# Optimization experiments

Measured on AMD Instinct MI355X. Metric: run time of the kernel, lower is better.

## Reference

```python
import jax, jax.numpy as jnp
import numpy as np

T = 4096
D_MODEL = 1024
H = 16          # n_heads
HD = 64         # head_dim = d_model // n_heads
LW = 64         # local_window
LT = 16         # latent_tokens
CHUNK = 32      # remote_chunk_size


def setup_inputs() -> dict:
    key = jax.random.key(0)
    ks = jax.random.split(key, 11)
    s = 0.02
    return {
        "x":  jax.random.normal(ks[0], (T, D_MODEL), dtype=jnp.float32),
        "Wq": jax.random.normal(ks[1], (D_MODEL, D_MODEL), dtype=jnp.float32) * s,
        "bq": jnp.zeros((D_MODEL,), dtype=jnp.float32),
        "Wk": jax.random.normal(ks[2], (D_MODEL, D_MODEL), dtype=jnp.float32) * s,
        "bk": jnp.zeros((D_MODEL,), dtype=jnp.float32),
        "Wv": jax.random.normal(ks[3], (D_MODEL, D_MODEL), dtype=jnp.float32) * s,
        "bv": jnp.zeros((D_MODEL,), dtype=jnp.float32),
        "Wo": jax.random.normal(ks[4], (D_MODEL, D_MODEL), dtype=jnp.float32) * s,
        "bo": jnp.zeros((D_MODEL,), dtype=jnp.float32),
        "Wg": jax.random.normal(ks[5], (H, D_MODEL), dtype=jnp.float32) * s,
        "bg": jnp.zeros((H,), dtype=jnp.float32),
    }


def reference(x, Wq, bq, Wk, bk, Wv, bv, Wo, bo, Wg, bg):
    """Runs prefill: forward_step for each token, returning per-step outputs [T, D_MODEL].

    Local cache = circular FIFO of size LW (append + pop-oldest == ring overwrite;
    softmax is permutation-invariant so slot order is irrelevant).
    Evicted tokens accumulate in pending sums; every CHUNK evictions the mean k/v
    is written into the remote latent ring of size LT (oldest overwritten).
    Attention happens BEFORE appending the current token's k/v, matching the torch code.
    """
    scale = 1.0 / np.sqrt(HD)
    Tn = x.shape[0]
    Q = (x @ Wq.T + bq).reshape(Tn, H, HD)
    K = (x @ Wk.T + bk).reshape(Tn, H, HD)
    V = (x @ Wv.T + bv).reshape(Tn, H, HD)
    G = jax.nn.sigmoid(x @ Wg.T + bg)  # [T, H] simple gate

    z = lambda *s: jnp.zeros(s, dtype=x.dtype)
    init = (z(LW, H, HD), z(LW, H, HD),   # local k/v ring
            z(LT, H, HD), z(LT, H, HD),   # remote k/v ring
            z(H, HD), z(H, HD),           # pending k/v sums
            jnp.int32(0), jnp.int32(0))   # pending count, remote count

    def step(carry, inp):
        lk, lv, rk, rv, pks, pvs, pc, rc = carry
        q, k, v, g, t = inp
        # ---- local attention over filled slots (count = min(t, LW)) ----
        lvalid = jnp.arange(LW) < jnp.minimum(t, LW)
        ls = jnp.einsum('hd,nhd->hn', q, lk) * scale
        ls = jnp.where(lvalid[None, :], ls, -1e30)
        lo = jnp.einsum('hn,nhd->hd', jax.nn.softmax(ls, axis=-1), lv)
        lo = lo * (t > 0)
        # ---- remote (compressed latent) attention ----
        rvalid = jnp.arange(LT) < jnp.minimum(rc, LT)
        rs = jnp.einsum('hd,nhd->hn', q, rk) * scale
        rs = jnp.where(rvalid[None, :], rs, -1e30)
        ro = jnp.einsum('hn,nhd->hd', jax.nn.softmax(rs, axis=-1), rv)
        ro = ro * (rc > 0)
        # ---- gate and combine ----
        gate = g[:, None]
        out = gate * lo + (1.0 - gate) * ro  # [H, HD]
        # ---- append k/v: ring write evicts token t-LW into pending ----
        pos = jnp.mod(t, LW)
        evict = (t >= LW)
        pks = pks + jnp.where(evict, lk[pos], 0.0)
        pvs = pvs + jnp.where(evict, lv[pos], 0.0)
        pc = pc + evict.astype(jnp.int32)
        lk = lk.at[pos].set(k)
        lv = lv.at[pos].set(v)
        # ---- compress pending into remote ring when CHUNK reached ----
        comp = (pc == CHUNK)
        ridx = jnp.mod(rc, LT)
        rk = jnp.where(comp, rk.at[ridx].set(pks / CHUNK), rk)
        rv = jnp.where(comp, rv.at[ridx].set(pvs / CHUNK), rv)
        rc = rc + comp.astype(jnp.int32)
        pks = jnp.where(comp, 0.0, pks)
        pvs = jnp.where(comp, 0.0, pvs)
        pc = jnp.where(comp, 0, pc)
        return (lk, lv, rk, rv, pks, pvs, pc, rc), out

    ts = jnp.arange(Tn, dtype=jnp.int32)
    _, outs = jax.lax.scan(step, init, (Q, K, V, G, ts))
    return outs.reshape(Tn, D_MODEL) @ Wo.T + bo
```

## Files before the change

kernel.cpp:

```cpp
#include <hip/hip_runtime.h>
#include <hip/hip_bf16.h>
#include <math.h>

typedef __attribute__((ext_vector_type(8))) short short8;
typedef __attribute__((ext_vector_type(4))) float f32x4;

#define TT 4096
#define DM 1024
#define NH 16
#define HD 64
#define PSTR 168

typedef __attribute__((address_space(3))) unsigned int lds_u32;
typedef __attribute__((address_space(1))) unsigned int glb_u32;

__device__ __forceinline__ void async_cp16(const void* g, void* l) {
    __builtin_amdgcn_global_load_lds((glb_u32*)g, (lds_u32*)l, 16, 0, 0);
}

__device__ __forceinline__ float bf2f(unsigned short u) {
    union { unsigned int i; float f; } v;
    v.i = (unsigned int)u << 16;
    return v.f;
}

__global__ __launch_bounds__(256) void cast_all(
    const float* __restrict__ x,  const float* __restrict__ wq,
    const float* __restrict__ wk, const float* __restrict__ wv,
    const float* __restrict__ wo, const float* __restrict__ wg,
    __hip_bfloat16* __restrict__ xb,  __hip_bfloat16* __restrict__ wqb,
    __hip_bfloat16* __restrict__ wkb, __hip_bfloat16* __restrict__ wvb,
    __hip_bfloat16* __restrict__ wob, __hip_bfloat16* __restrict__ wgb)
{
    int b = blockIdx.x;
    const float* src;
    __hip_bfloat16* dst;
    size_t base;
    if (b < 4096)      { src = x;  dst = xb;  base = (size_t)b * 1024; }
    else if (b < 5120) { src = wq; dst = wqb; base = (size_t)(b - 4096) * 1024; }
    else if (b < 6144) { src = wk; dst = wkb; base = (size_t)(b - 5120) * 1024; }
    else if (b < 7168) { src = wv; dst = wvb; base = (size_t)(b - 6144) * 1024; }
    else if (b < 8192) { src = wo; dst = wob; base = (size_t)(b - 7168) * 1024; }
    else               { src = wg; dst = wgb; base = (size_t)(b - 8192) * 1024; }
    size_t i = base + (size_t)threadIdx.x * 4;
    float4 v = *(const float4*)(src + i);
    __hip_bfloat16 h0 = (__hip_bfloat16)v.x;
    __hip_bfloat16 h1 = (__hip_bfloat16)v.y;
    __hip_bfloat16 h2 = (__hip_bfloat16)v.z;
    __hip_bfloat16 h3 = (__hip_bfloat16)v.w;
    ushort4 u;
    u.x = *(unsigned short*)&h0;
    u.y = *(unsigned short*)&h1;
    u.z = *(unsigned short*)&h2;
    u.w = *(unsigned short*)&h3;
    *(ushort4*)((unsigned short*)dst + i) = u;
}

template <typename OutT>
__global__ __launch_bounds__(512, 2) void gemm256(
    const __hip_bfloat16* __restrict__ A,
    const __hip_bfloat16* __restrict__ B0, const __hip_bfloat16* __restrict__ B1,
    const __hip_bfloat16* __restrict__ B2,
    const float* __restrict__ c0, const float* __restrict__ c1, const float* __restrict__ c2,
    OutT* __restrict__ O0, OutT* __restrict__ O1, OutT* __restrict__ O2)
{
    const int K  = DM;
    const int NT = 16;
    __shared__ __align__(16) unsigned short sL[2][4][128 * 64];

    const int grp = blockIdx.y >> 2;
    const __hip_bfloat16* B = grp == 0 ? B0 : (grp == 1 ? B1 : B2);
    const float* bias       = grp == 0 ? c0 : (grp == 1 ? c1 : c2);
    OutT* O                 = grp == 0 ? O0 : (grp == 1 ? O1 : O2);

    const int tid  = threadIdx.x;
    const int w    = tid >> 6;
    const int lane = tid & 63;
    const int l16  = lane & 15;
    const int quad = lane >> 4;
    const int wr   = w >> 2;
    const int wc   = w & 3;
    const int rowBase = blockIdx.x * 256;
    const int colBase = (blockIdx.y & 3) * 256;

    const int srow = lane >> 3;
    const int schk = (lane & 7) ^ srow;
    const __hip_bfloat16* gA = A + (size_t)(rowBase + w * 8 + srow) * K + schk * 8;
    const __hip_bfloat16* gB = B + (size_t)(colBase + w * 8 + srow) * K + schk * 8;
    const int dstoff = w * 8 * 64;

#define STG(buf, slot, gbase, half, kt) do {                                                   \
    async_cp16((gbase) + (size_t)((half) * 128)      * K + (kt) * 64, &sL[buf][slot][dstoff]); \
    async_cp16((gbase) + (size_t)((half) * 128 + 64) * K + (kt) * 64, &sL[buf][slot][64 * 64 + dstoff]); \
} while (0)

    const int cs0 = ((quad)     ^ (l16 & 7)) * 8;
    const int cs1 = ((4 + quad) ^ (l16 & 7)) * 8;

    f32x4 acc[8][4];
#pragma unroll
    for (int i = 0; i < 8; ++i)
#pragma unroll
        for (int j = 0; j < 4; ++j) acc[i][j] = (f32x4){0.f, 0.f, 0.f, 0.f};

    STG(0, 2, gB, 0, 0); STG(0, 3, gB, 1, 0); STG(0, 0, gA, 0, 0); STG(0, 1, gA, 1, 0);
    STG(1, 2, gB, 0, 1); STG(1, 3, gB, 1, 1); STG(1, 0, gA, 0, 1);

    short8 af[4][2], bf[4][2];
    for (int t = 0; t < NT; ++t) {
        const int b = t & 1;
        const unsigned short* pa = &sL[b][wr][0];
        const unsigned short* pb = &sL[b][2 + (wc >> 1)][(wc & 1) * 64 * 64];

        if (t == NT - 1) asm volatile("s_waitcnt vmcnt(0)" ::: "memory");
        else             asm volatile("s_waitcnt vmcnt(6)" ::: "memory");
        __builtin_amdgcn_s_barrier();
#pragma unroll
        for (int m = 0; m < 4; ++m) {
            af[m][0] = *(const short8*)&pa[(m * 16 + l16) * 64 + cs0];
            af[m][1] = *(const short8*)&pa[(m * 16 + l16) * 64 + cs1];
        }
#pragma unroll
        for (int n = 0; n < 2; ++n) {
            bf[n][0] = *(const short8*)&pb[(n * 16 + l16) * 64 + cs0];
            bf[n][1] = *(const short8*)&pb[(n * 16 + l16) * 64 + cs1];
        }
        if (t + 1 < NT) STG(b ^ 1, 1, gA, 1, t + 1);
        asm volatile("s_waitcnt lgkmcnt(0)" ::: "memory");
        __builtin_amdgcn_sched_barrier(0);
        __builtin_amdgcn_s_setprio(1);
#pragma unroll
        for (int ks = 0; ks < 2; ++ks)
#pragma unroll
            for (int m = 0; m < 4; ++m)
#pragma unroll
                for (int n = 0; n < 2; ++n)
                    acc[m][n] = __builtin_amdgcn_mfma_f32_16x16x32_bf16(af[m][ks], bf[n][ks], acc[m][n], 0, 0, 0);
        __builtin_amdgcn_s_setprio(0);

#pragma unroll
        for (int n = 2; n < 4; ++n) {
            bf[n][0] = *(const short8*)&pb[(n * 16 + l16) * 64 + cs0];
            bf[n][1] = *(const short8*)&pb[(n * 16 + l16) * 64 + cs1];
        }
        asm volatile("s_waitcnt lgkmcnt(0)" ::: "memory");
        __builtin_amdgcn_sched_barrier(0);
        __builtin_amdgcn_s_setprio(1);
#pragma unroll
        for (int ks = 0; ks < 2; ++ks)
#pragma unroll
            for (int m = 0; m < 4; ++m)
#pragma unroll
            for (int n = 2; n < 4; ++n)
                acc[m][n] = __builtin_amdgcn_mfma_f32_16x16x32_bf16(af[m][ks], bf[n][ks], acc[m][n], 0, 0, 0);
        __builtin_amdgcn_s_setprio(0);
        __builtin_amdgcn_s_barrier();

#pragma unroll
        for (int m = 0; m < 4; ++m) {
            af[m][0] = *(const short8*)&pa[((m + 4) * 16 + l16) * 64 + cs0];
            af[m][1] = *(const short8*)&pa[((m + 4) * 16 + l16) * 64 + cs1];
        }
        if (t + 2 < NT) STG(b, 2, gB, 0, t + 2);
        asm volatile("s_waitcnt lgkmcnt(0)" ::: "memory");
        __builtin_amdgcn_sched_barrier(0);
        __builtin_amdgcn_s_setprio(1);
#pragma unroll
        for (int ks = 0; ks < 2; ++ks)
#pragma unroll
            for (int m = 0; m < 4; ++m)
#pragma unroll
                for (int n = 0; n < 2; ++n)
                    acc[m + 4][n] = __builtin_amdgcn_mfma_f32_16x16x32_bf16(af[m][ks], bf[n][ks], acc[m + 4][n], 0, 0, 0);
        __builtin_amdgcn_s_setprio(0);
        __builtin_amdgcn_s_barrier();

        if (t + 2 < NT) { STG(b, 3, gB, 1, t + 2); STG(b, 0, gA, 0, t + 2); }
        __builtin_amdgcn_s_setprio(1);
#pragma unroll
        for (int ks = 0; ks < 2; ++ks)
#pragma unroll
            for (int m = 0; m < 4; ++m)
#pragma unroll
            for (int n = 2; n < 4; ++n)
                acc[m + 4][n] = __builtin_amdgcn_mfma_f32_16x16x32_bf16(af[m][ks], bf[n][ks], acc[m + 4][n], 0, 0, 0);
        __builtin_amdgcn_s_setprio(0);
    }
#undef STG

#pragma unroll
    for (int n = 0; n < 4; ++n) {
        int col = colBase + wc * 64 + n * 16 + l16;
        float bv = bias[col];
#pragma unroll
        for (int m = 0; m < 8; ++m) {
#pragma unroll
            for (int r = 0; r < 4; ++r) {
                int row = rowBase + wr * 128 + m * 16 + quad * 4 + r;
                O[(size_t)row * DM + col] = (OutT)(acc[m][n][r] + bv);
            }
        }
    }
}

template <typename OutT>
__global__ __launch_bounds__(256) void gemm_n64(
    const __hip_bfloat16* __restrict__ A,
    const __hip_bfloat16* __restrict__ B,
    const float* __restrict__ bias,
    OutT* __restrict__ O)
{
    const int K = DM;
    const int NT = 32;
    __shared__ __align__(16) unsigned short sA[2 * 128 * 32];
    __shared__ __align__(16) unsigned short sB[2 * 64 * 32];

    const int tid  = threadIdx.x;
    const int w    = tid >> 6;
    const int lane = tid & 63;
    const int l16  = lane & 15;
    const int quad = lane >> 4;
    const int rowBase = blockIdx.x * 128;
    const int colBase = blockIdx.y * 64;

    const int srow   = lane >> 2;
    const int sswz   = (srow & 3) ^ (srow >> 2);
    const int gchunk = (lane & 3) ^ sswz;
    const __hip_bfloat16* gA = A + (size_t)(rowBase + w * 32 + srow) * K + gchunk * 8;
    const __hip_bfloat16* gB = B + (size_t)(colBase + w * 16 + srow) * K + gchunk * 8;
    unsigned short* lA0 = sA + w * 32 * 32;
    unsigned short* lB0 = sB + w * 16 * 32;

    const int fswz = (l16 & 3) ^ (l16 >> 2);
    const int mrow = w * 32;

    f32x4 acc[2][4];
#pragma unroll
    for (int i = 0; i < 2; ++i)
#pragma unroll
        for (int j = 0; j < 4; ++j) acc[i][j] = (f32x4){0.f, 0.f, 0.f, 0.f};

    async_cp16(gA,                  lA0);
    async_cp16(gA + (size_t)16 * K, lA0 + 16 * 32);
    async_cp16(gB,                  lB0);
    async_cp16(gA + 32,                  lA0 + 128 * 32);
    async_cp16(gA + 32 + (size_t)16 * K, lA0 + 128 * 32 + 16 * 32);
    async_cp16(gB + 32,                  lB0 + 64 * 32);

    for (int t = 0; t < NT; ++t) {
        if (t == NT - 1) asm volatile("s_waitcnt vmcnt(0)" ::: "memory");
        else             asm volatile("s_waitcnt vmcnt(3)" ::: "memory");
        __builtin_amdgcn_s_barrier();

        const unsigned short* pA = sA + (t & 1) * (128 * 32);
        const unsigned short* pB = sB + (t & 1) * (64 * 32);
        short8 af[2], bf[4];
#pragma unroll
        for (int mt = 0; mt < 2; ++mt)
            af[mt] = *(const short8*)&pA[(mrow + mt * 16 + l16) * 32 + (quad ^ fswz) * 8];
#pragma unroll
        for (int nt = 0; nt < 4; ++nt)
            bf[nt] = *(const short8*)&pB[(nt * 16 + l16) * 32 + (quad ^ fswz) * 8];
        asm volatile("s_waitcnt lgkmcnt(0)" ::: "memory");
        __builtin_amdgcn_sched_barrier(0);
        __builtin_amdgcn_s_barrier();

        if (t + 2 < NT) {
            const int k2 = (t + 2) * 32;
            unsigned short* dA = lA0 + (t & 1) * (128 * 32);
            unsigned short* dB = lB0 + (t & 1) * (64 * 32);
            async_cp16(gA + k2,                  dA);
            async_cp16(gA + k2 + (size_t)16 * K, dA + 16 * 32);
            async_cp16(gB + k2,                  dB);
        }

#pragma unroll
        for (int mt = 0; mt < 2; ++mt)
#pragma unroll
            for (int nt = 0; nt < 4; ++nt)
                acc[mt][nt] = __builtin_amdgcn_mfma_f32_16x16x32_bf16(af[mt], bf[nt], acc[mt][nt], 0, 0, 0);
    }

#pragma unroll
    for (int nt = 0; nt < 4; ++nt) {
        int col = colBase + nt * 16 + l16;
        float bv = bias[col];
#pragma unroll
        for (int mt = 0; mt < 2; ++mt) {
#pragma unroll
            for (int r = 0; r < 4; ++r) {
                int row = rowBase + mrow + mt * 16 + quad * 4 + r;
                O[(size_t)row * DM + col] = (OutT)(acc[mt][nt][r] + bv);
            }
        }
    }
}

__global__ __launch_bounds__(256) void aux_kernel(
    const __hip_bfloat16* __restrict__ K,
    const __hip_bfloat16* __restrict__ V,
    const __hip_bfloat16* __restrict__ xb,
    const __hip_bfloat16* __restrict__ Wgb,
    const float* __restrict__ bg,
    __hip_bfloat16* __restrict__ CK,
    __hip_bfloat16* __restrict__ CV,
    float* __restrict__ G)
{
    const int b = blockIdx.x;
    if (b < 256) {
        const int c  = b >> 1;
        const int d0 = (b & 1) * 512 + threadIdx.x * 2;
        const unsigned short* Ku = (const unsigned short*)K;
        const unsigned short* Vu = (const unsigned short*)V;
        float ak0 = 0.f, ak1 = 0.f, av0 = 0.f, av1 = 0.f;
#pragma unroll 8
        for (int i = 0; i < 32; ++i) {
            size_t off = (size_t)(c * 32 + i) * DM + d0;
            ushort2 kv = *(const ushort2*)(Ku + off);
            ushort2 vv = *(const ushort2*)(Vu + off);
            ak0 += bf2f(kv.x); ak1 += bf2f(kv.y);
            av0 += bf2f(vv.x); av1 += bf2f(vv.y);
        }
        __hip_bfloat16 k0 = (__hip_bfloat16)(ak0 * (1.f / 32.f));
        __hip_bfloat16 k1 = (__hip_bfloat16)(ak1 * (1.f / 32.f));
        __hip_bfloat16 v0 = (__hip_bfloat16)(av0 * (1.f / 32.f));
        __hip_bfloat16 v1 = (__hip_bfloat16)(av1 * (1.f / 32.f));
        ushort2 ko, vo;
        ko.x = *(unsigned short*)&k0; ko.y = *(unsigned short*)&k1;
        vo.x = *(unsigned short*)&v0; vo.y = *(unsigned short*)&v1;
        *(ushort2*)((unsigned short*)CK + (size_t)c * DM + d0) = ko;
        *(ushort2*)((unsigned short*)CV + (size_t)c * DM + d0) = vo;
        return;
    }
    const int unit = threadIdx.x >> 6;
    const int lane = threadIdx.x & 63;
    const int l16  = lane & 15;
    const int quad = lane >> 4;
    const int t0   = (b - 256) * 64 + unit * 16;
    const __hip_bfloat16* ap = xb  + (size_t)(t0 + l16) * DM + quad * 8;
    const __hip_bfloat16* bp = Wgb + (size_t)l16 * DM + quad * 8;
    f32x4 acc = (f32x4){0.f, 0.f, 0.f, 0.f};
#pragma unroll 4
    for (int k0 = 0; k0 < DM; k0 += 32) {
        short8 a = *(const short8*)(ap + k0);
        short8 bb = *(const short8*)(bp + k0);
        acc = __builtin_amdgcn_mfma_f32_16x16x32_bf16(a, bb, acc, 0, 0, 0);
    }
    float bgv = bg[l16];
#pragma unroll
    for (int r = 0; r < 4; ++r) {
        int t = t0 + quad * 4 + r;
        float z = acc[r] + bgv;
        G[t * NH + l16] = 1.f / (1.f + __expf(-z));
    }
}

__global__ __launch_bounds__(256) void attn_mfma(
    const __hip_bfloat16* __restrict__ Q,
    const __hip_bfloat16* __restrict__ K,
    const __hip_bfloat16* __restrict__ V,
    const __hip_bfloat16* __restrict__ CK,
    const __hip_bfloat16* __restrict__ CV,
    const float* __restrict__ G,
    __hip_bfloat16* __restrict__ Aout)
{
    __shared__ alignas(16) unsigned short Pls[64 * PSTR];
    __shared__ alignas(16) unsigned short Vts[64 * PSTR];

    const int h   = blockIdx.y;
    const int t0  = blockIdx.x * 64;
    const int tid = threadIdx.x;
    const int w    = tid >> 6;
    const int lane = tid & 63;
    const int l16  = lane & 15;
    const int quad = lane >> 4;
    const float scale = 0.125f;

    const int rc0  = (t0 >= 96) ? ((t0 - 64) >> 5) : 0;
    const int cmin = rc0 > 16 ? rc0 - 16 : 0;

    const unsigned short* Vu  = (const unsigned short*)V;
    const unsigned short* CVu = (const unsigned short*)CV;

    {
#pragma unroll
        for (int gg = 0; gg < 2; ++gg) {
            const int g = w * 2 + gg;
#pragma unroll
            for (int i = 0; i < 2; ++i) {
                const int pair = lane + 64 * i;
                if (pair < 80) {
                    const int j = pair * 2;
                    const unsigned short *s0, *s1;
                    if (j < 128) {
                        int tok0 = t0 - 64 + j; if (tok0 < 0) tok0 = 0;
                        int tok1 = t0 - 63 + j; if (tok1 < 0) tok1 = 0;
                        s0 = Vu + (size_t)tok0 * DM + h * 64 + g * 8;
                        s1 = Vu + (size_t)tok1 * DM + h * 64 + g * 8;
                    } else {
                        int c0 = cmin + (j - 128); if (c0 > 127) c0 = 127;
                        int c1 = c0 + 1;           if (c1 > 127) c1 = 127;
                        s0 = CVu + (size_t)c0 * DM + h * 64 + g * 8;
                        s1 = CVu + (size_t)c1 * DM + h * 64 + g * 8;
                    }
                    short8 v0 = *(const short8*)s0;
                    short8 v1 = *(const short8*)s1;
#pragma unroll
                    for (int e = 0; e < 8; ++e) {
                        ushort2 pk;
                        pk.x = (unsigned short)v0[e];
                        pk.y = (unsigned short)v1[e];
                        *(ushort2*)&Vts[(g * 8 + e) * PSTR + j] = pk;
                    }
                }
            }
        }
    }

    const __hip_bfloat16* qp = Q + (size_t)(t0 + w * 16 + l16) * DM + h * 64 + quad * 8;
    short8 qf0 = *(const short8*)(qp);
    short8 qf1 = *(const short8*)(qp + 32);

    f32x4 sc[8];
#pragma unroll
    for (int jt = 0; jt < 8; ++jt) {
        int j = jt * 16 + l16;
        int tok = t0 - 64 + j;
        tok = tok < 0 ? 0 : tok;
        const __hip_bfloat16* kp = K + (size_t)tok * DM + h * 64 + quad * 8;
        short8 b0 = *(const short8*)(kp);
        short8 b1 = *(const short8*)(kp + 32);
        f32x4 a = __builtin_amdgcn_mfma_f32_16x16x32_bf16(qf0, b0, (f32x4){0.f,0.f,0.f,0.f}, 0, 0, 0);
        sc[jt]  = __builtin_amdgcn_mfma_f32_16x16x32_bf16(qf1, b1, a, 0, 0, 0);
    }
    f32x4 sc2[2];
#pragma unroll
    for (int jt = 0; jt < 2; ++jt) {
        int c = cmin + jt * 16 + l16;
        if (c > 127) c = 127;
        const __hip_bfloat16* cp = CK + (size_t)c * DM + h * 64 + quad * 8;
        short8 b0 = *(const short8*)(cp);
        short8 b1 = *(const short8*)(cp + 32);
        f32x4 a = __builtin_amdgcn_mfma_f32_16x16x32_bf16(qf0, b0, (f32x4){0.f,0.f,0.f,0.f}, 0, 0, 0);
        sc2[jt] = __builtin_amdgcn_mfma_f32_16x16x32_bf16(qf1, b1, a, 0, 0, 0);
    }

    __syncthreads();

    const int rbase = w * 16 + quad * 4;
    float gl[4], g2[4];
    float mx[4], sm[4], mx2[4], sm2[4];
#pragma unroll
    for (int reg = 0; reg < 4; ++reg) {
        int rr = rbase + reg;
        int t  = t0 + rr;
        float g = G[t * NH + h];
        int rc = (t >= 96) ? ((t - 64) >> 5) : 0;
        gl[reg] = (t > 0)  ? g        : 0.f;
        g2[reg] = (rc > 0) ? (1.f - g) : 0.f;

        int jlo = rr > (64 - t0) ? rr : (64 - t0);
        int jhi = rr + 63;
        float m = -1e30f;
#pragma unroll
        for (int jt = 0; jt < 8; ++jt) {
            int j = jt * 16 + l16;
            float s = (j >= jlo && j <= jhi) ? sc[jt][reg] * scale : -1e30f;
            sc[jt][reg] = s;
            m = fmaxf(m, s);
        }
        mx[reg] = m;

        int nvis = rc < 16 ? rc : 16;
        int clo = rc - nvis, chi = rc - 1;
        float m2 = -1e30f;
#pragma unroll
        for (int jt = 0; jt < 2; ++jt) {
            int c = cmin + jt * 16 + l16;
            float s = (c >= clo && c <= chi) ? sc2[jt][reg] * scale : -1e30f;
            sc2[jt][reg] = s;
            m2 = fmaxf(m2, s);
        }
        mx2[reg] = m2;
    }
#pragma unroll
    for (int off = 1; off <= 8; off <<= 1)
#pragma unroll
        for (int reg = 0; reg < 4; ++reg) {
            mx[reg]  = fmaxf(mx[reg],  __shfl_xor(mx[reg],  off));
            mx2[reg] = fmaxf(mx2[reg], __shfl_xor(mx2[reg], off));
        }
#pragma unroll
    for (int reg = 0; reg < 4; ++reg) {
        float s = 0.f, s2 = 0.f;
#pragma unroll
        for (int jt = 0; jt < 8; ++jt) {
            float p = __expf(sc[jt][reg] - mx[reg]);
            sc[jt][reg] = p;
            s += p;
        }
#pragma unroll
        for (int jt = 0; jt < 2; ++jt) {
            float p = __expf(sc2[jt][reg] - mx2[reg]);
            sc2[jt][reg] = p;
            s2 += p;
        }
        sm[reg] = s; sm2[reg] = s2;
    }
#pragma unroll
    for (int off = 1; off <= 8; off <<= 1)
#pragma unroll
        for (int reg = 0; reg < 4; ++reg) {
            sm[reg]  += __shfl_xor(sm[reg],  off);
            sm2[reg] += __shfl_xor(sm2[reg], off);
        }

#pragma unroll
    for (int reg = 0; reg < 4; ++reg) {
        float f1 = gl[reg] / sm[reg];
        float f2 = g2[reg] / sm2[reg];
        int rowoff = (rbase + reg) * PSTR;
#pragma unroll
        for (int jt = 0; jt < 8; ++jt) {
            __hip_bfloat16 hb = (__hip_bfloat16)(sc[jt][reg] * f1);
            Pls[rowoff + jt * 16 + l16] = *(unsigned short*)&hb;
        }
#pragma unroll
        for (int jt = 0; jt < 2; ++jt) {
            __hip_bfloat16 hb = (__hip_bfloat16)(sc2[jt][reg] * f2);
            Pls[rowoff + 128 + jt * 16 + l16] = *(unsigned short*)&hb;
        }
    }
    asm volatile("s_waitcnt lgkmcnt(0)" ::: "memory");

    f32x4 o[4];
#pragma unroll
    for (int nt = 0; nt < 4; ++nt) o[nt] = (f32x4){0.f, 0.f, 0.f, 0.f};
#pragma unroll
    for (int kt = 0; kt < 5; ++kt) {
        short8 a = *(const short8*)&Pls[(w * 16 + l16) * PSTR + kt * 32 + quad * 8];
#pragma unroll
        for (int nt = 0; nt < 4; ++nt) {
            int dd = nt * 16 + l16;
            short8 b = *(const short8*)&Vts[dd * PSTR + kt * 32 + quad * 8];
            o[nt] = __builtin_amdgcn_mfma_f32_16x16x32_bf16(a, b, o[nt], 0, 0, 0);
        }
    }

#pragma unroll
    for (int nt = 0; nt < 4; ++nt) {
#pragma unroll
        for (int reg = 0; reg < 4; ++reg) {
            int row = t0 + rbase + reg;
            int col = h * 64 + nt * 16 + l16;
            Aout[(size_t)row * DM + col] = (__hip_bfloat16)(o[nt][reg]);
        }
    }
}

extern "C" void kernel_launch(void* const* d_in, const int* in_sizes, int n_in,
                              void* d_out, int out_size, void* d_ws, size_t ws_size,
                              hipStream_t stream)
{
    const float* x  = (const float*)d_in[0];
    const float* Wq = (const float*)d_in[1];
    const float* bq = (const float*)d_in[2];
    const float* Wk = (const float*)d_in[3];
    const float* bk = (const float*)d_in[4];
    const float* Wv = (const float*)d_in[5];
    const float* bv = (const float*)d_in[6];
    const float* Wo = (const float*)d_in[7];
    const float* bo = (const float*)d_in[8];
    const float* Wg = (const float*)d_in[9];
    const float* bg = (const float*)d_in[10];
    float* out = (float*)d_out;

    char* ws = (char*)d_ws;
    const size_t MB = 1024 * 1024;
    __hip_bfloat16* xb  = (__hip_bfloat16*)(ws + 0 * MB);
    __hip_bfloat16* Qb  = (__hip_bfloat16*)(ws + 8 * MB);
    __hip_bfloat16* Kb  = (__hip_bfloat16*)(ws + 16 * MB);
    __hip_bfloat16* Vb  = (__hip_bfloat16*)(ws + 24 * MB);
    __hip_bfloat16* Ab  = (__hip_bfloat16*)(ws + 32 * MB);
    __hip_bfloat16* Wqb = (__hip_bfloat16*)(ws + 40 * MB);
    __hip_bfloat16* Wkb = (__hip_bfloat16*)(ws + 42 * MB);
    __hip_bfloat16* Wvb = (__hip_bfloat16*)(ws + 44 * MB);
    __hip_bfloat16* Wob = (__hip_bfloat16*)(ws + 46 * MB);
    __hip_bfloat16* CKb = (__hip_bfloat16*)(ws + 48 * MB);
    __hip_bfloat16* CVb = (__hip_bfloat16*)(ws + 48 * MB + 256*1024);
    float* Gf           = (float*)(ws + 48 * MB + 512 * 1024);
    __hip_bfloat16* Wgb = (__hip_bfloat16*)(ws + 48 * MB + 768*1024);

    cast_all<<<dim3(8208), 256, 0, stream>>>(x, Wq, Wk, Wv, Wo, Wg,
                                             xb, Wqb, Wkb, Wvb, Wob, Wgb);

    gemm256<__hip_bfloat16><<<dim3(16, 12), 512, 0, stream>>>(
        xb, Wqb, Wkb, Wvb, bq, bk, bv, Qb, Kb, Vb);
    aux_kernel<<<dim3(320), 256, 0, stream>>>(Kb, Vb, xb, Wgb, bg, CKb, CVb, Gf);
    attn_mfma<<<dim3(64, 16), 256, 0, stream>>>(Qb, Kb, Vb, CKb, CVb, Gf, Ab);
    gemm_n64<float><<<dim3(32, 16), 256, 0, stream>>>(Ab, Wob, bo, out);
}
```

Measured before the change: 177.4 us.

## Retile fused QKV GEMM to 256x192 tiles over concatenated weights

The QKV projection GEMM now treats Wq/Wk/Wv as one concatenated 3072-row weight and uses 256x192 output tiles, giving a 16x16 grid of 256 blocks instead of 16x12 (192 blocks). That is meant to fill the GPU's compute units more evenly. The LDS staging is reorganised into seven 64-row slots, and the barrier and prefetch schedule is adjusted to match. The change relies on Wq/Wk/Wv and Q/K/V being contiguous in the workspace (2MB and 8MB strides), which holds for the existing layout. The epilogue picks the bias and output slice per column.

```diff
diff --git a/kernel.cpp b/kernel.cpp
--- a/kernel.cpp
+++ b/kernel.cpp
@@ -57,21 +57,15 @@
 }
 
 template <typename OutT>
-__global__ __launch_bounds__(512, 2) void gemm256(
+__global__ __launch_bounds__(512, 2) void gemm192(
     const __hip_bfloat16* __restrict__ A,
-    const __hip_bfloat16* __restrict__ B0, const __hip_bfloat16* __restrict__ B1,
-    const __hip_bfloat16* __restrict__ B2,
+    const __hip_bfloat16* __restrict__ Bcat,
     const float* __restrict__ c0, const float* __restrict__ c1, const float* __restrict__ c2,
-    OutT* __restrict__ O0, OutT* __restrict__ O1, OutT* __restrict__ O2)
+    OutT* __restrict__ Ocat)
 {
     const int K  = DM;
     const int NT = 16;
-    __shared__ __align__(16) unsigned short sL[2][4][128 * 64];
-
-    const int grp = blockIdx.y >> 2;
-    const __hip_bfloat16* B = grp == 0 ? B0 : (grp == 1 ? B1 : B2);
-    const float* bias       = grp == 0 ? c0 : (grp == 1 ? c1 : c2);
-    OutT* O                 = grp == 0 ? O0 : (grp == 1 ? O1 : O2);
+    __shared__ __align__(16) unsigned short sL[2][7][64 * 64];
 
     const int tid  = threadIdx.x;
     const int w    = tid >> 6;
@@ -81,51 +75,52 @@
     const int wr   = w >> 2;
     const int wc   = w & 3;
     const int rowBase = blockIdx.x * 256;
-    const int colBase = (blockIdx.y & 3) * 256;
-
-    const int srow = lane >> 3;
-    const int schk = (lane & 7) ^ srow;
-    const __hip_bfloat16* gA = A + (size_t)(rowBase + w * 8 + srow) * K + schk * 8;
-    const __hip_bfloat16* gB = B + (size_t)(colBase + w * 8 + srow) * K + schk * 8;
-    const int dstoff = w * 8 * 64;
-
-#define STG(buf, slot, gbase, half, kt) do {                                                   \
-    async_cp16((gbase) + (size_t)((half) * 128)      * K + (kt) * 64, &sL[buf][slot][dstoff]); \
-    async_cp16((gbase) + (size_t)((half) * 128 + 64) * K + (kt) * 64, &sL[buf][slot][64 * 64 + dstoff]); \
-} while (0)
+    const int colBase = blockIdx.y * 192;
+
+    const int srow8 = tid >> 3;
+    const int schk  = (tid & 7) ^ (srow8 & 7);
+    const __hip_bfloat16* gA = A    + (size_t)(rowBase + srow8) * K + schk * 8;
+    const __hip_bfloat16* gB = Bcat + (size_t)(colBase + srow8) * K + schk * 8;
+    const int ldst = w * 512;
+
+#define STGA(buf, ua, kt) async_cp16(gA + (size_t)(ua) * 64 * K + (kt) * 64, &sL[buf][ua][ldst])
+#define STGB(buf, ub, kt) async_cp16(gB + (size_t)(ub) * 64 * K + (kt) * 64, &sL[buf][4 + (ub)][ldst])
 
     const int cs0 = ((quad)     ^ (l16 & 7)) * 8;
     const int cs1 = ((4 + quad) ^ (l16 & 7)) * 8;
 
-    f32x4 acc[8][4];
+    f32x4 acc[8][3];
 #pragma unroll
     for (int i = 0; i < 8; ++i)
 #pragma unroll
-        for (int j = 0; j < 4; ++j) acc[i][j] = (f32x4){0.f, 0.f, 0.f, 0.f};
-
-    STG(0, 2, gB, 0, 0); STG(0, 3, gB, 1, 0); STG(0, 0, gA, 0, 0); STG(0, 1, gA, 1, 0);
-    STG(1, 2, gB, 0, 1); STG(1, 3, gB, 1, 1); STG(1, 0, gA, 0, 1);
-
-    short8 af[4][2], bf[4][2];
+        for (int j = 0; j < 3; ++j) acc[i][j] = (f32x4){0.f, 0.f, 0.f, 0.f};
+
+    STGB(0, 0, 0); STGB(0, 1, 0); STGB(0, 2, 0);
+    STGA(0, 0, 0); STGA(0, 2, 0); STGA(0, 1, 0); STGA(0, 3, 0);
+    STGB(1, 0, 1); STGB(1, 1, 1); STGB(1, 2, 1);
+    STGA(1, 0, 1); STGA(1, 2, 1); STGA(1, 1, 1); STGA(1, 3, 1);
+
+    short8 af[4][2], bf[3][2];
     for (int t = 0; t < NT; ++t) {
         const int b = t & 1;
-        const unsigned short* pa = &sL[b][wr][0];
-        const unsigned short* pb = &sL[b][2 + (wc >> 1)][(wc & 1) * 64 * 64];
+        const unsigned short* paL = &sL[b][wr * 2][0];
+        const unsigned short* paH = &sL[b][wr * 2 + 1][0];
 
         if (t == NT - 1) asm volatile("s_waitcnt vmcnt(0)" ::: "memory");
-        else             asm volatile("s_waitcnt vmcnt(6)" ::: "memory");
+        else             asm volatile("s_waitcnt vmcnt(7)" ::: "memory");
         __builtin_amdgcn_s_barrier();
 #pragma unroll
         for (int m = 0; m < 4; ++m) {
-            af[m][0] = *(const short8*)&pa[(m * 16 + l16) * 64 + cs0];
-            af[m][1] = *(const short8*)&pa[(m * 16 + l16) * 64 + cs1];
-        }
-#pragma unroll
-        for (int n = 0; n < 2; ++n) {
-            bf[n][0] = *(const short8*)&pb[(n * 16 + l16) * 64 + cs0];
-            bf[n][1] = *(const short8*)&pb[(n * 16 + l16) * 64 + cs1];
-        }
-        if (t + 1 < NT) STG(b ^ 1, 1, gA, 1, t + 1);
+            af[m][0] = *(const short8*)&paL[(m * 16 + l16) * 64 + cs0];
+            af[m][1] = *(const short8*)&paL[(m * 16 + l16) * 64 + cs1];
+        }
+        {
+            const int bu  = (wc * 48) >> 6;
+            const int bro = (wc * 48) & 63;
+            const unsigned short* pb = &sL[b][4 + bu][0];
+            bf[0][0] = *(const short8*)&pb[(bro + l16) * 64 + cs0];
+            bf[0][1] = *(const short8*)&pb[(bro + l16) * 64 + cs1];
+        }
         asm volatile("s_waitcnt lgkmcnt(0)" ::: "memory");
         __builtin_amdgcn_sched_barrier(0);
         __builtin_amdgcn_s_setprio(1);
@@ -133,71 +128,78 @@
         for (int ks = 0; ks < 2; ++ks)
 #pragma unroll
             for (int m = 0; m < 4; ++m)
-#pragma unroll
-                for (int n = 0; n < 2; ++n)
+                acc[m][0] = __builtin_amdgcn_mfma_f32_16x16x32_bf16(af[m][ks], bf[0][ks], acc[m][0], 0, 0, 0);
+        __builtin_amdgcn_s_setprio(0);
+
+#pragma unroll
+        for (int n = 1; n < 3; ++n) {
+            const int bu  = (wc * 48 + n * 16) >> 6;
+            const int bro = (wc * 48 + n * 16) & 63;
+            const unsigned short* pb = &sL[b][4 + bu][0];
+            bf[n][0] = *(const short8*)&pb[(bro + l16) * 64 + cs0];
+            bf[n][1] = *(const short8*)&pb[(bro + l16) * 64 + cs1];
+        }
+        asm volatile("s_waitcnt lgkmcnt(0)" ::: "memory");
+        __builtin_amdgcn_sched_barrier(0);
+        __builtin_amdgcn_s_barrier();
+        if (t + 2 < NT) {
+            STGB(b, 0, t + 2); STGB(b, 1, t + 2); STGB(b, 2, t + 2);
+            STGA(b, 0, t + 2); STGA(b, 2, t + 2);
+        }
+        __builtin_amdgcn_s_setprio(1);
+#pragma unroll
+        for (int ks = 0; ks < 2; ++ks)
+#pragma unroll
+            for (int m = 0; m < 4; ++m)
+#pragma unroll
+                for (int n = 1; n < 3; ++n)
                     acc[m][n] = __builtin_amdgcn_mfma_f32_16x16x32_bf16(af[m][ks], bf[n][ks], acc[m][n], 0, 0, 0);
         __builtin_amdgcn_s_setprio(0);
 
 #pragma unroll
-        for (int n = 2; n < 4; ++n) {
-            bf[n][0] = *(const short8*)&pb[(n * 16 + l16) * 64 + cs0];
-            bf[n][1] = *(const short8*)&pb[(n * 16 + l16) * 64 + cs1];
+        for (int m = 0; m < 4; ++m) {
+            af[m][0] = *(const short8*)&paH[(m * 16 + l16) * 64 + cs0];
+            af[m][1] = *(const short8*)&paH[(m * 16 + l16) * 64 + cs1];
         }
         asm volatile("s_waitcnt lgkmcnt(0)" ::: "memory");
         __builtin_amdgcn_sched_barrier(0);
+        __builtin_amdgcn_s_barrier();
+        if (t + 2 < NT) { STGA(b, 1, t + 2); STGA(b, 3, t + 2); }
         __builtin_amdgcn_s_setprio(1);
 #pragma unroll
         for (int ks = 0; ks < 2; ++ks)
 #pragma unroll
             for (int m = 0; m < 4; ++m)
-#pragma unroll
-            for (int n = 2; n < 4; ++n)
-                acc[m][n] = __builtin_amdgcn_mfma_f32_16x16x32_bf16(af[m][ks], bf[n][ks], acc[m][n], 0, 0, 0);
+                acc[m + 4][0] = __builtin_amdgcn_mfma_f32_16x16x32_bf16(af[m][ks], bf[0][ks], acc[m + 4][0], 0, 0, 0);
         __builtin_amdgcn_s_setprio(0);
-        __builtin_amdgcn_s_barrier();
-
-#pragma unroll
-        for (int m = 0; m < 4; ++m) {
-            af[m][0] = *(const short8*)&pa[((m + 4) * 16 + l16) * 64 + cs0];
-            af[m][1] = *(const short8*)&pa[((m + 4) * 16 + l16) * 64 + cs1];
-        }
-        if (t + 2 < NT) STG(b, 2, gB, 0, t + 2);
-        asm volatile("s_waitcnt lgkmcnt(0)" ::: "memory");
-        __builtin_amdgcn_sched_barrier(0);
+
         __builtin_amdgcn_s_setprio(1);
 #pragma unroll
         for (int ks = 0; ks < 2; ++ks)
 #pragma unroll
             for (int m = 0; m < 4; ++m)
 #pragma unroll
-                for (int n = 0; n < 2; ++n)
+                for (int n = 1; n < 3; ++n)
                     acc[m + 4][n] = __builtin_amdgcn_mfma_f32_16x16x32_bf16(af[m][ks], bf[n][ks], acc[m + 4][n], 0, 0, 0);
         __builtin_amdgcn_s_setprio(0);
-        __builtin_amdgcn_s_barrier();
-
-        if (t + 2 < NT) { STG(b, 3, gB, 1, t + 2); STG(b, 0, gA, 0, t + 2); }
-        __builtin_amdgcn_s_setprio(1);
-#pragma unroll
-        for (int ks = 0; ks < 2; ++ks)
-#pragma unroll
-            for (int m = 0; m < 4; ++m)
-#pragma unroll
-            for (int n = 2; n < 4; ++n)
-                acc[m + 4][n] = __builtin_amdgcn_mfma_f32_16x16x32_bf16(af[m][ks], bf[n][ks], acc[m + 4][n], 0, 0, 0);
-        __builtin_amdgcn_s_setprio(0);
-    }
-#undef STG
-
-#pragma unroll
-    for (int n = 0; n < 4; ++n) {
-        int col = colBase + wc * 64 + n * 16 + l16;
-        float bv = bias[col];
+    }
+#undef STGA
+#undef STGB
+
+#pragma unroll
+    for (int n = 0; n < 3; ++n) {
+        int col = colBase + wc * 48 + n * 16 + l16;
+        int grp = col >> 10;
+        int cl  = col & 1023;
+        const float* bias = grp == 0 ? c0 : (grp == 1 ? c1 : c2);
+        float bv = bias[cl];
+        OutT* O = Ocat + (size_t)grp * TT * DM;
 #pragma unroll
         for (int m = 0; m < 8; ++m) {
 #pragma unroll
             for (int r = 0; r < 4; ++r) {
                 int row = rowBase + wr * 128 + m * 16 + quad * 4 + r;
-                O[(size_t)row * DM + col] = (OutT)(acc[m][n][r] + bv);
+                O[(size_t)row * DM + cl] = (OutT)(acc[m][n][r] + bv);
             }
         }
     }
@@ -594,8 +596,8 @@
     cast_all<<<dim3(8208), 256, 0, stream>>>(x, Wq, Wk, Wv, Wo, Wg,
                                              xb, Wqb, Wkb, Wvb, Wob, Wgb);
 
-    gemm256<__hip_bfloat16><<<dim3(16, 12), 512, 0, stream>>>(
-        xb, Wqb, Wkb, Wvb, bq, bk, bv, Qb, Kb, Vb);
+    gemm192<__hip_bfloat16><<<dim3(16, 16), 512, 0, stream>>>(
+        xb, Wqb, bq, bk, bv, Qb);
     aux_kernel<<<dim3(320), 256, 0, stream>>>(Kb, Vb, xb, Wgb, bg, CKb, CVb, Gf);
     attn_mfma<<<dim3(64, 16), 256, 0, stream>>>(Qb, Kb, Vb, CKb, CVb, Gf, Ab);
     gemm_n64<float><<<dim3(32, 16), 256, 0, stream>>>(Ab, Wob, bo, out);
```

After: 176.3 us. Within noise of the previous version (-0.6%).
